# Performance work log

Hardware: AMD Instinct MI355X
Metric: run time of the kernel (lower is better)

## Reference

```python
import jax, jax.numpy as jnp
import numpy as np

DIM = 1024
NUM_HEADS = 16
HEAD_DIM = DIM // NUM_HEADS
SCALE = HEAD_DIM ** -0.5


def setup_inputs() -> dict:
    key = jax.random.key(0)
    k1, k2, k3 = jax.random.split(key, 3)
    B, N = 2, 2048
    x = jax.random.normal(k1, (B, N, DIM), dtype=jnp.float32)
    W_qkv = jax.random.normal(k2, (DIM, 3 * DIM), dtype=jnp.float32) * (DIM ** -0.5)
    b_qkv = jnp.zeros((3 * DIM,), dtype=jnp.float32)
    W_proj = jax.random.normal(k3, (DIM, DIM), dtype=jnp.float32) * (DIM ** -0.5)
    b_proj = jnp.zeros((DIM,), dtype=jnp.float32)
    return {"x": x, "W_qkv": W_qkv, "b_qkv": b_qkv, "W_proj": W_proj, "b_proj": b_proj}


def reference(x, W_qkv, b_qkv, W_proj, b_proj):
    B, N, D = x.shape
    qkv = x @ W_qkv + b_qkv                      # [B, N, 3D]
    qkv = qkv.reshape(B, N, 3, NUM_HEADS, HEAD_DIM)
    qkv = jnp.transpose(qkv, (2, 0, 3, 1, 4))    # [3, B, H, N, hd]
    q, k, v = qkv[0], qkv[1], qkv[2]
    attn = jnp.einsum('bhqd,bhkd->bhqk', q, k) * SCALE  # [B, H, N, N]
    attn = jax.nn.softmax(attn, axis=-1)
    out = jnp.einsum('bhqk,bhkd->bhqd', attn, v)        # [B, H, N, hd]
    out = jnp.transpose(out, (0, 2, 1, 3)).reshape(B, N, D)
    out = out @ W_proj + b_proj
    return out
```

## Files before the change

kernel.cpp:

```cpp
#include <hip/hip_runtime.h>


typedef __bf16 bf16_t;
typedef __bf16 bf16x2 __attribute__((ext_vector_type(2)));
typedef __bf16 bf16x4 __attribute__((ext_vector_type(4)));
typedef __bf16 bf16x8 __attribute__((ext_vector_type(8)));
typedef float  f32x4  __attribute__((ext_vector_type(4)));

#define NTOK 2048
#define DIM  1024
#define NH   16
#define HD   64
#define SCL2 0.18033688011112042f

#define MFMA16(a, b, c) __builtin_amdgcn_mfma_f32_16x16x32_bf16((a), (b), (c), 0, 0, 0)
#define BAR()   __builtin_amdgcn_s_barrier()
#define LGKM0() asm volatile("s_waitcnt lgkmcnt(0)" ::: "memory")

__device__ __forceinline__ void gload_lds16(const void* g, void* l) {
  __builtin_amdgcn_global_load_lds((const __attribute__((address_space(1))) void*)g,
                                   (__attribute__((address_space(3))) void*)l, 16, 0, 0);
}

__device__ __forceinline__ void transpose_cvt_tile(const float* __restrict__ W,
                                                   bf16_t* __restrict__ WT,
                                                   int cols, int bx, int by) {
  __shared__ float tile[32][33];
  int j0 = bx * 32, i0 = by * 32;
  int c = threadIdx.x & 31, r0 = threadIdx.x >> 5;
#pragma unroll
  for (int it = 0; it < 4; ++it) {
    int r = r0 + it * 8;
    tile[r][c] = W[(long)(i0 + r) * cols + j0 + c];
  }
  __syncthreads();
  int orl = threadIdx.x >> 3, sub = threadIdx.x & 7;
  int orow = j0 + orl;
  bf16x4 v;
#pragma unroll
  for (int u = 0; u < 4; ++u) v[u] = (bf16_t)tile[sub * 4 + u][orl];
  int chunk_g = (i0 >> 3) + (sub >> 1);
  *(bf16x4*)(WT + (long)orow * 1024 + ((chunk_g ^ (orow & 7)) << 3) + (sub & 1) * 4) = v;
}

__global__ __launch_bounds__(256) void k_prep(const float* __restrict__ x,
                                              bf16_t* __restrict__ xb,
                                              const float* __restrict__ Wq,
                                              bf16_t* __restrict__ WqT,
                                              const float* __restrict__ Wp,
                                              bf16_t* __restrict__ WpT) {
  int id = blockIdx.x;
  if (id < 2048) {
    int i = (id * 256 + threadIdx.x) * 8;
    float4 a = *(const float4*)(x + i);
    float4 b = *(const float4*)(x + i + 4);
    bf16x8 v;
    v[0] = (bf16_t)a.x; v[1] = (bf16_t)a.y; v[2] = (bf16_t)a.z; v[3] = (bf16_t)a.w;
    v[4] = (bf16_t)b.x; v[5] = (bf16_t)b.y; v[6] = (bf16_t)b.z; v[7] = (bf16_t)b.w;
    int r = i >> 10, c = (i & 1023) >> 3;
    *(bf16x8*)(xb + r * 1024 + ((c ^ (r & 7)) << 3)) = v;
  } else if (id < 2048 + 3072) {
    int t = id - 2048;
    transpose_cvt_tile(Wq, WqT, 3072, t % 96, t / 96);
  } else {
    int t = id - 5120;
    transpose_cvt_tile(Wp, WpT, 1024, t & 31, t >> 5);
  }
}

__global__ __launch_bounds__(512, 2) void k_gemm_qkv(const bf16_t* __restrict__ xb,
                                                     const bf16_t* __restrict__ WqT,
                                                     const float* __restrict__ bq,
                                                     bf16_t* __restrict__ Qb,
                                                     bf16_t* __restrict__ Kb,
                                                     bf16_t* __restrict__ Vt) {
  __shared__ alignas(16) bf16_t SH[57344];
  const int t = threadIdx.x;
  const int w = t >> 6, lane = t & 63;
  const int l15 = lane & 15, g = lane >> 4;
  const int wm = w >> 2, wn = w & 3;
  const int xr = l15 & 7;

  const int bid = blockIdx.x;
  const int xcd = bid & 7, ib = bid >> 3;
  const int bm = ((xcd & 3) * 4 + (ib & 3)) * 256;
  const int bn = ((xcd >> 2) * 8 + (ib >> 2)) * 192;

  const bf16_t* Ag = xb + (long)bm * 1024;
  const bf16_t* Bg = WqT + (long)bn * 1024;

  auto Asl = [&](int slot) -> bf16_t* { return SH + slot * 16384; };
  auto Bsl = [&](int slot) -> bf16_t* { return SH + 32768 + slot * 12288; };

  auto st1 = [&](bf16_t* lds, const bf16_t* gsrc, int row0, int kt) {
    gload_lds16(gsrc + (long)(row0 + (t >> 3)) * 1024 + kt * 64 + (t & 7) * 8,
                (char*)lds + row0 * 128 + t * 16);
  };
  auto evA0 = [&](int slot, int kt) {
    st1(Asl(slot), Ag, 0, kt);
    st1(Asl(slot), Ag, 128, kt);
  };
  auto evA1 = [&](int slot, int kt) {
    st1(Asl(slot), Ag, 64, kt);
    st1(Asl(slot), Ag, 192, kt);
  };
  auto evB = [&](int slot, int kt) {
    st1(Bsl(slot), Bg, 0, kt);
    st1(Bsl(slot), Bg, 64, kt);
    st1(Bsl(slot), Bg, 128, kt);
  };

  f32x4 acc[8][3];
  const f32x4 vzero = {0.f, 0.f, 0.f, 0.f};
#pragma unroll
  for (int m = 0; m < 8; ++m)
#pragma unroll
    for (int n = 0; n < 3; ++n) acc[m][n] = vzero;

  bf16x8 bf[3][2], af[4][2];
  auto ldBn = [&](int slot, int n) {
#pragma unroll
    for (int kk = 0; kk < 2; ++kk)
      bf[n][kk] = *(const bf16x8*)((const char*)Bsl(slot) +
                  (wn * 48 + n * 16 + l15) * 128 + (((kk * 4 + g) ^ xr) << 4));
  };
  auto ldA = [&](int slot, int half) {
#pragma unroll
    for (int m = 0; m < 4; ++m)
#pragma unroll
      for (int kk = 0; kk < 2; ++kk)
        af[m][kk] = *(const bf16x8*)((const char*)Asl(slot) +
                    (wm * 128 + half * 64 + m * 16 + l15) * 128 +
                    (((kk * 4 + g) ^ xr) << 4));
  };
  auto mma2 = [&](int mb) {
    __builtin_amdgcn_s_setprio(1);
#pragma unroll
    for (int m = 0; m < 4; ++m)
#pragma unroll
      for (int n = 0; n < 2; ++n)
#pragma unroll
        for (int kk = 0; kk < 2; ++kk)
          acc[mb + m][n] = MFMA16(af[m][kk], bf[n][kk], acc[mb + m][n]);
    __builtin_amdgcn_s_setprio(0);
  };
  auto mma1 = [&](int mb) {
    __builtin_amdgcn_s_setprio(1);
#pragma unroll
    for (int m = 0; m < 4; ++m)
#pragma unroll
      for (int kk = 0; kk < 2; ++kk)
        acc[mb + m][2] = MFMA16(af[m][kk], bf[2][kk], acc[mb + m][2]);
    __builtin_amdgcn_s_setprio(0);
  };

  evB(0, 0); evA0(0, 0); evA1(0, 0);
  evB(1, 1); evA0(1, 1);
  asm volatile("s_waitcnt vmcnt(5)" ::: "memory");
  BAR();

  for (int T = 0; T < 16; ++T) {
    const int h = T & 1;
    const bool stg = (T + 2) < 16;
    if (T + 1 < 16) evA1(h ^ 1, T + 1);
    ldBn(h, 0); ldBn(h, 1); ldA(h, 0);
    BAR(); LGKM0();
    mma2(0);
    BAR();
    ldBn(h, 2);
    BAR(); LGKM0();
    mma1(0);
    BAR();
    ldA(h, 1);
    if (stg) evB(h, T + 2);
    BAR(); LGKM0();
    mma2(4);
    BAR();
    if (stg) {
      evA0(h, T + 2);
      asm volatile("s_waitcnt vmcnt(5)" ::: "memory");
    } else {
      asm volatile("s_waitcnt vmcnt(0)" ::: "memory");
    }
    BAR();
    mma1(4);
    BAR();
  }

  const int bb = bm >> 11;
  const int tok0 = bm & 2047;
#pragma unroll
  for (int n = 0; n < 3; ++n) {
    int lc = wn * 48 + n * 16 + l15;
    int col = bn + lc;
    int t3 = col >> 10;
    int d = col & 63;
    int region = lc >> 6;
    float bias = bq[col];
#pragma unroll
    for (int m = 0; m < 8; ++m) {
#pragma unroll
      for (int r = 0; r < 4; ++r) {
        int ltok = wm * 128 + m * 16 + g * 4 + r;
        float val = acc[m][n][r] + bias;
        int off;
        if (t3 == 0) {
          off = ltok * 64 + d;
          val *= SCL2;
        } else if (t3 == 1) {
          int rr = ltok & 63;
          off = (ltok >> 6) * 4096 + rr * 64 + (((d >> 3) ^ (rr & 7)) << 3) + (d & 7);
        } else {
          int ct = ltok & 63;
          off = (ltok >> 6) * 4096 + d * 64 + (((ct >> 3) ^ (d & 7)) << 3) + (ct & 7);
        }
        SH[region * 16384 + off] = (bf16_t)val;
      }
    }
  }
  BAR();
#pragma unroll
  for (int hl = 0; hl < 3; ++hl) {
    int col0 = bn + hl * 64;
    int t3 = col0 >> 10;
    int hh = (col0 >> 6) & 15;
    bf16_t* dst = (t3 == 0) ? Qb : (t3 == 1 ? Kb : Vt);
    long tilebase = (t3 == 0) ? (long)tok0 * HD : (long)(tok0 >> 6) * 4096;
    long gbase = (long)(bb * NH + hh) * (NTOK * HD) + tilebase;
#pragma unroll
    for (int p = 0; p < 4; ++p) {
      bf16x8 vv = *(const bf16x8*)(SH + hl * 16384 + p * 4096 + t * 8);
      *(bf16x8*)(dst + gbase + p * 4096 + t * 8) = vv;
    }
  }
}

__device__ __forceinline__ void gemm_core(const bf16_t* __restrict__ A,
                                          const bf16_t* __restrict__ B,
                                          int K, int bm, int bn,
                                          bf16_t* As, bf16_t* Bs, f32x4 acc[4][4]) {
  const int t = threadIdx.x;
  const int lane = t & 63;
  const int w = t >> 6;
  const int wr = (w >> 1) * 64, wc = (w & 1) * 64;
  const int l15 = lane & 15, g = lane >> 4;
  const int srow = t >> 3, scol = (t & 7) * 8;
  const f32x4 vzero = {0.f, 0.f, 0.f, 0.f};
#pragma unroll
  for (int m = 0; m < 4; ++m)
#pragma unroll
    for (int n = 0; n < 4; ++n) acc[m][n] = vzero;

  const bf16_t* ga = A + (long)(bm + srow) * K + scol;
  const bf16_t* gb = B + (long)(bn + srow) * K + scol;
  bf16_t* lA = As + srow * 64 + scol;
  bf16_t* lB = Bs + srow * 64 + scol;
  const int xr = l15 & 7;

  auto stageAB = [&](int buf, int k0) {
#pragma unroll
    for (int j = 0; j < 4; ++j) {
      gload_lds16(ga + (long)32 * j * K + k0, lA + buf * 8192 + j * 2048);
      gload_lds16(gb + (long)32 * j * K + k0, lB + buf * 8192 + j * 2048);
    }
  };

  const int nsteps = K >> 6;
  stageAB(0, 0);
  stageAB(1, 64);

  for (int s = 0; s < nsteps; ++s) {
    if (s == nsteps - 1) asm volatile("s_waitcnt vmcnt(0)" ::: "memory");
    else                 asm volatile("s_waitcnt vmcnt(8)" ::: "memory");
    __builtin_amdgcn_s_barrier();
    const char* Ab = (const char*)(As + (s & 1) * 8192);
    const char* Bb = (const char*)(Bs + (s & 1) * 8192);
#pragma unroll
    for (int kk = 0; kk < 2; ++kk) {
      bf16x8 af[4], bfv[4];
#pragma unroll
      for (int m = 0; m < 4; ++m)
        af[m] = *(const bf16x8*)(Ab + (wr + m * 16 + l15) * 128 +
                                 (((kk * 4 + g) ^ xr) << 4));
#pragma unroll
      for (int n = 0; n < 4; ++n)
        bfv[n] = *(const bf16x8*)(Bb + (wc + n * 16 + l15) * 128 +
                                  (((kk * 4 + g) ^ xr) << 4));
#pragma unroll
      for (int m = 0; m < 4; ++m)
#pragma unroll
        for (int n = 0; n < 4; ++n)
          acc[m][n] = MFMA16(af[m], bfv[n], acc[m][n]);
    }
    __builtin_amdgcn_s_barrier();
    if (s + 2 < nsteps) stageAB(s & 1, (s + 2) * 64);
  }
}

__global__ __launch_bounds__(256, 3) void k_attn(const bf16_t* __restrict__ Qb,
                                                 const bf16_t* __restrict__ Kb,
                                                 const bf16_t* __restrict__ Vt,
                                                 bf16_t* __restrict__ Ob) {
  __shared__ alignas(16) bf16_t Ks[2][64 * 64];
  __shared__ alignas(16) bf16_t Vs[2][64 * 64];
  __shared__ alignas(16) char  P2[4][4096];

  const int b0 = blockIdx.x;
  const int swz = (b0 & 7) * 64 + (b0 >> 3);
  const int qt = swz & 15, bh = swz >> 4;
  const int b = bh >> 4, h = bh & 15;
  const int t = threadIdx.x;
  const int w = t >> 6, lane = t & 63;
  const int l15 = lane & 15, g = lane >> 4;
  const bf16_t* Qp = Qb + bh * (NTOK * HD);
  const bf16_t* Kp = Kb + bh * (NTOK * HD);
  const bf16_t* Vp = Vt + bh * (NTOK * HD);
  const int q0 = qt * 128 + w * 32;
  char* P2w = &P2[w][0];

  const int cs0 = ((g ^ (l15 & 7)) << 4);
  const int cs1 = cs0 ^ 64;

  bf16x8 qfr[2][2];
#pragma unroll
  for (int qf = 0; qf < 2; ++qf)
#pragma unroll
    for (int kk = 0; kk < 2; ++kk)
      qfr[qf][kk] = *(const bf16x8*)(Qp + (q0 + qf * 16 + l15) * HD + kk * 32 + g * 8);

  bf16x8 ones;
#pragma unroll
  for (int i = 0; i < 8; ++i) ones[i] = (bf16_t)1.0f;

  const f32x4 vzero = {0.f, 0.f, 0.f, 0.f};
  f32x4 o[2][4];
#pragma unroll
  for (int qf = 0; qf < 2; ++qf)
#pragma unroll
    for (int df = 0; df < 4; ++df) o[qf][df] = vzero;
  f32x4 o_sum[2] = {vzero, vzero};

  auto stage = [&](int buf, int tile) {
    const bf16_t* gk = Kp + tile * 4096 + t * 8;
    const bf16_t* gv = Vp + tile * 4096 + t * 8;
    gload_lds16(gk,        (char*)Ks[buf] + t * 16);
    gload_lds16(gk + 2048, (char*)Ks[buf] + 4096 + t * 16);
    gload_lds16(gv,        (char*)Vs[buf] + t * 16);
    gload_lds16(gv + 2048, (char*)Vs[buf] + 4096 + t * 16);
  };

  stage(0, 0);
  stage(1, 1);

  for (int i = 0; i < 32; ++i) {
    if (i == 31) asm volatile("s_waitcnt vmcnt(0)" ::: "memory");
    else         asm volatile("s_waitcnt vmcnt(4)" ::: "memory");
    __builtin_amdgcn_s_barrier();
    const char* kbuf = (const char*)Ks[i & 1];
    const char* vbuf = (const char*)Vs[i & 1];
    f32x4 s[2][4];
    __builtin_amdgcn_s_setprio(1);
#pragma unroll
    for (int kf = 0; kf < 4; ++kf) {
      int rb = (kf * 16 + l15) * 128;
      bf16x8 ka0 = *(const bf16x8*)(kbuf + rb + cs0);
      bf16x8 ka1 = *(const bf16x8*)(kbuf + rb + cs1);
      s[0][kf] = MFMA16(ka0, qfr[0][0], vzero);
      s[1][kf] = MFMA16(ka0, qfr[1][0], vzero);
      s[0][kf] = MFMA16(ka1, qfr[0][1], s[0][kf]);
      s[1][kf] = MFMA16(ka1, qfr[1][1], s[1][kf]);
    }
    __builtin_amdgcn_s_setprio(0);
#pragma unroll
    for (int qf = 0; qf < 2; ++qf)
#pragma unroll
      for (int kf = 0; kf < 4; ++kf) {
        bf16x4 pw;
        pw[0] = (bf16_t)__builtin_amdgcn_exp2f(s[qf][kf][0]);
        pw[1] = (bf16_t)__builtin_amdgcn_exp2f(s[qf][kf][1]);
        pw[2] = (bf16_t)__builtin_amdgcn_exp2f(s[qf][kf][2]);
        pw[3] = (bf16_t)__builtin_amdgcn_exp2f(s[qf][kf][3]);
        *(bf16x4*)(P2w + qf * 2048 + (2 * kf + (g >> 1)) * 256 + l15 * 16 + 8 * (g & 1)) = pw;
      }
    __builtin_amdgcn_s_setprio(1);
#pragma unroll
    for (int kb = 0; kb < 2; ++kb) {
      bf16x8 pf0 = *(const bf16x8*)(P2w + kb * 1024 + lane * 16);
      bf16x8 pf1 = *(const bf16x8*)(P2w + 2048 + kb * 1024 + lane * 16);
      int csk = kb ? cs1 : cs0;
      o_sum[0] = MFMA16(ones, pf0, o_sum[0]);
      o_sum[1] = MFMA16(ones, pf1, o_sum[1]);
#pragma unroll
      for (int df = 0; df < 4; ++df) {
        bf16x8 va = *(const bf16x8*)(vbuf + (df * 16 + l15) * 128 + csk);
        o[0][df] = MFMA16(va, pf0, o[0][df]);
        o[1][df] = MFMA16(va, pf1, o[1][df]);
      }
    }
    __builtin_amdgcn_s_setprio(0);
    __builtin_amdgcn_s_barrier();
    if (i + 2 < 32) stage(i & 1, i + 2);
  }
#pragma unroll
  for (int qf = 0; qf < 2; ++qf) {
    float inv = 1.0f / o_sum[qf][0];
    int tok = q0 + qf * 16 + l15;
    bf16_t* oprow = Ob + (long)(b * NTOK + tok) * DIM;
    const int xr = l15 & 7;
#pragma unroll
    for (int df = 0; df < 4; ++df) {
#pragma unroll
      for (int rp = 0; rp < 2; ++rp) {
        bf16x2 v2;
        v2[0] = (bf16_t)(o[qf][df][rp * 2]     * inv);
        v2[1] = (bf16_t)(o[qf][df][rp * 2 + 1] * inv);
        int c = h * 8 + df * 2 + (g >> 1);
        *(bf16x2*)(oprow + ((c ^ xr) << 3) + (g & 1) * 4 + rp * 2) = v2;
      }
    }
  }
}

__global__ __launch_bounds__(256) void k_gemm_proj(const bf16_t* __restrict__ Ob,
                                                   const bf16_t* __restrict__ WpT,
                                                   const float* __restrict__ bp,
                                                   float* __restrict__ out) {
  __shared__ alignas(16) bf16_t As[2 * 128 * 64];
  __shared__ alignas(16) bf16_t Bs[2 * 128 * 64];
  f32x4 acc[4][4];
  const int bid = blockIdx.x;
  const int bn = (bid & 7) * 128;
  const int bm = (bid >> 3) * 128;
  gemm_core(Ob, WpT, DIM, bm, bn, As, Bs, acc);

  const int lane = threadIdx.x & 63, w = threadIdx.x >> 6;
  const int wr = (w >> 1) * 64, wc = (w & 1) * 64;
  const int l15 = lane & 15, g = lane >> 4;
#pragma unroll
  for (int n = 0; n < 4; ++n) {
    int col = bn + wc + n * 16 + l15;
    float bias = bp[col];
#pragma unroll
    for (int m = 0; m < 4; ++m) {
      int rowb = bm + wr + m * 16 + g * 4;
#pragma unroll
      for (int r = 0; r < 4; ++r)
        out[(long)(rowb + r) * DIM + col] = acc[m][n][r] + bias;
    }
  }
}

extern "C" void kernel_launch(void* const* d_in, const int* in_sizes, int n_in,
                              void* d_out, int out_size, void* d_ws, size_t ws_size,
                              hipStream_t stream) {
  const float* x     = (const float*)d_in[0];
  const float* Wqkv  = (const float*)d_in[1];
  const float* bqkv  = (const float*)d_in[2];
  const float* Wproj = (const float*)d_in[3];
  const float* bproj = (const float*)d_in[4];
  float* out = (float*)d_out;

  char* ws = (char*)d_ws;
  bf16_t* xb  = (bf16_t*)(ws);
  bf16_t* WqT = (bf16_t*)(ws + (8l  << 20));
  bf16_t* WpT = (bf16_t*)(ws + (14l << 20));
  bf16_t* Qb  = (bf16_t*)(ws + (16l << 20));
  bf16_t* Kb  = (bf16_t*)(ws + (24l << 20));
  bf16_t* Vt  = (bf16_t*)(ws + (32l << 20));
  bf16_t* Ob  = (bf16_t*)(ws);

  k_prep<<<6144, 256, 0, stream>>>(x, xb, Wqkv, WqT, Wproj, WpT);
  k_gemm_qkv<<<256, 512, 0, stream>>>(xb, WqT, bqkv, Qb, Kb, Vt);
  k_attn<<<512, 256, 0, stream>>>(Qb, Kb, Vt, Ob);
  k_gemm_proj<<<256, 256, 0, stream>>>(Ob, WpT, bproj, out);
}
```

Measured before the change: 105.1 us.

## Load V tiles directly from global into registers, drop V LDS staging

The attention kernel no longer stages V tiles through shared memory. Each wave reads its V fragments straight from global memory into registers at the top of each iteration, and the vmcnt waits are adjusted for the K-only pipeline. Removing the V buffers frees LDS, and the launch bound is raised from 3 to 4 blocks per SM to allow more occupancy. In exchange, every wave fetches the whole V tile redundantly from global/L2, those loads are not overlapped by the double buffer, and more registers are used.

```diff
diff --git a/kernel.cpp b/kernel.cpp
--- a/kernel.cpp
+++ b/kernel.cpp
@@ -297,12 +297,11 @@
   }
 }
 
-__global__ __launch_bounds__(256, 3) void k_attn(const bf16_t* __restrict__ Qb,
+__global__ __launch_bounds__(256, 4) void k_attn(const bf16_t* __restrict__ Qb,
                                                  const bf16_t* __restrict__ Kb,
                                                  const bf16_t* __restrict__ Vt,
                                                  bf16_t* __restrict__ Ob) {
   __shared__ alignas(16) bf16_t Ks[2][64 * 64];
-  __shared__ alignas(16) bf16_t Vs[2][64 * 64];
   __shared__ alignas(16) char  P2[4][4096];
 
   const int b0 = blockIdx.x;
@@ -318,7 +317,8 @@
   const int q0 = qt * 128 + w * 32;
   char* P2w = &P2[w][0];
 
-  const int cs0 = ((g ^ (l15 & 7)) << 4);
+  const int xr7 = l15 & 7;
+  const int cs0 = ((g ^ xr7) << 4);
   const int cs1 = cs0 ^ 64;
 
   bf16x8 qfr[2][2];
@@ -340,24 +340,28 @@
     for (int df = 0; df < 4; ++df) o[qf][df] = vzero;
   f32x4 o_sum[2] = {vzero, vzero};
 
-  auto stage = [&](int buf, int tile) {
+  auto stageK = [&](int buf, int tile) {
     const bf16_t* gk = Kp + tile * 4096 + t * 8;
-    const bf16_t* gv = Vp + tile * 4096 + t * 8;
     gload_lds16(gk,        (char*)Ks[buf] + t * 16);
     gload_lds16(gk + 2048, (char*)Ks[buf] + 4096 + t * 16);
-    gload_lds16(gv,        (char*)Vs[buf] + t * 16);
-    gload_lds16(gv + 2048, (char*)Vs[buf] + 4096 + t * 16);
-  };
-
-  stage(0, 0);
-  stage(1, 1);
+  };
+
+  stageK(0, 0);
+  stageK(1, 1);
 
   for (int i = 0; i < 32; ++i) {
-    if (i == 31) asm volatile("s_waitcnt vmcnt(0)" ::: "memory");
-    else         asm volatile("s_waitcnt vmcnt(4)" ::: "memory");
+    if (i >= 30) asm volatile("s_waitcnt vmcnt(0)" ::: "memory");
+    else         asm volatile("s_waitcnt vmcnt(2)" ::: "memory");
     __builtin_amdgcn_s_barrier();
     const char* kbuf = (const char*)Ks[i & 1];
-    const char* vbuf = (const char*)Vs[i & 1];
+    const bf16_t* vtile = Vp + i * 4096;
+    bf16x8 va[4][2];
+#pragma unroll
+    for (int df = 0; df < 4; ++df)
+#pragma unroll
+      for (int kb = 0; kb < 2; ++kb)
+        va[df][kb] = *(const bf16x8*)(vtile + (df * 16 + l15) * 64 +
+                                      (((kb * 4 + g) ^ xr7) << 3));
     f32x4 s[2][4];
     __builtin_amdgcn_s_setprio(1);
 #pragma unroll
@@ -387,26 +391,23 @@
     for (int kb = 0; kb < 2; ++kb) {
       bf16x8 pf0 = *(const bf16x8*)(P2w + kb * 1024 + lane * 16);
       bf16x8 pf1 = *(const bf16x8*)(P2w + 2048 + kb * 1024 + lane * 16);
-      int csk = kb ? cs1 : cs0;
       o_sum[0] = MFMA16(ones, pf0, o_sum[0]);
       o_sum[1] = MFMA16(ones, pf1, o_sum[1]);
 #pragma unroll
       for (int df = 0; df < 4; ++df) {
-        bf16x8 va = *(const bf16x8*)(vbuf + (df * 16 + l15) * 128 + csk);
-        o[0][df] = MFMA16(va, pf0, o[0][df]);
-        o[1][df] = MFMA16(va, pf1, o[1][df]);
+        o[0][df] = MFMA16(va[df][kb], pf0, o[0][df]);
+        o[1][df] = MFMA16(va[df][kb], pf1, o[1][df]);
       }
     }
     __builtin_amdgcn_s_setprio(0);
     __builtin_amdgcn_s_barrier();
-    if (i + 2 < 32) stage(i & 1, i + 2);
+    if (i + 2 < 32) stageK(i & 1, i + 2);
   }
 #pragma unroll
   for (int qf = 0; qf < 2; ++qf) {
     float inv = 1.0f / o_sum[qf][0];
     int tok = q0 + qf * 16 + l15;
     bf16_t* oprow = Ob + (long)(b * NTOK + tok) * DIM;
-    const int xr = l15 & 7;
 #pragma unroll
     for (int df = 0; df < 4; ++df) {
 #pragma unroll
@@ -415,7 +416,7 @@
         v2[0] = (bf16_t)(o[qf][df][rp * 2]     * inv);
         v2[1] = (bf16_t)(o[qf][df][rp * 2 + 1] * inv);
         int c = h * 8 + df * 2 + (g >> 1);
-        *(bf16x2*)(oprow + ((c ^ xr) << 3) + (g & 1) * 4 + rp * 2) = v2;
+        *(bf16x2*)(oprow + ((c ^ xr7) << 3) + (g & 1) * 4 + rp * 2) = v2;
       }
     }
   }
```

Measured after the change: 145.7 us. 1.39x slower.
